# Performance work log

Hardware: AMD Instinct MI355X
Metric: run time of the kernel (lower is better)

## Reference

```python
import jax, jax.numpy as jnp
import numpy as np

S = 16          # slice count (init kwarg)
EPS = 1e-5      # BN2d default eps


def markov_sub(m, s):
    """Vectorized get_markov_sub. m: [C, C] -> [s, C, C].
    ms[i][a,b] = where(m[i,b] > 0, m[a,b], 0); mss[k] = max over rows i in slice k.
    Equivalent closed form via per-column any/all positivity of the slice rows."""
    C = m.shape[0]
    pos = (m > 0.0).reshape(s, C // s, C)          # [s, slice_size, C]
    any_p = pos.any(axis=1)[:, None, :]            # [s, 1, C]
    all_p = pos.all(axis=1)[:, None, :]            # [s, 1, C]
    mb = m[None, :, :]                             # [1, C, C]
    return jnp.where(all_p, mb,
                     jnp.where(any_p, jnp.maximum(mb, 0.0), jnp.zeros_like(mb)))


def setup_inputs() -> dict:
    key = jax.random.key(0)
    ks = jax.random.split(key, 8)
    N, C, H, W = 4, 256, 32, 32
    s = S
    feats = jax.random.normal(ks[0], (N, C, H, W), jnp.float32)
    adj_matrix = jax.random.normal(ks[1], (N, C, C), jnp.float32)
    # three 1x1 conv layers: in = S*C, out = C (stacked on leading axis)
    conv_w = jax.random.normal(ks[2], (3, C, s * C), jnp.float32) / np.sqrt(s * C).astype(np.float32)
    conv_b = jax.random.normal(ks[3], (3, C), jnp.float32) * 0.01
    bn_gamma = jnp.ones((3, C), jnp.float32)
    bn_beta = jnp.zeros((3, C), jnp.float32)
    bn_mean = jax.random.normal(ks[4], (3, C), jnp.float32) * 0.1
    bn_var = jax.random.uniform(ks[5], (3, C), jnp.float32, minval=0.5, maxval=1.5)
    return {"feats": feats, "adj_matrix": adj_matrix, "conv_w": conv_w,
            "conv_b": conv_b, "bn_gamma": bn_gamma, "bn_beta": bn_beta,
            "bn_mean": bn_mean, "bn_var": bn_var}


def reference(feats, adj_matrix, conv_w, conv_b, bn_gamma, bn_beta, bn_mean, bn_var):
    N, C, H, W = feats.shape
    s = S
    # per-sample markov sub-adjacencies, computed once and reused across layers
    mss = jax.vmap(lambda m: markov_sub(m, s))(adj_matrix)      # [N, S, C, C]
    mss = mss.reshape(N, s * C, C)                              # [N, S*C, C]
    outs = []
    x = feats
    for l in range(3):
        xp = x.reshape(N, C, H * W)                             # [N, C, HW]
        y = jnp.einsum('nkc,ncp->nkp', mss, xp)                 # sparse.mm -> [N, S*C, HW]
        y = jnp.einsum('ok,nkp->nop', conv_w[l], y) + conv_b[l][None, :, None]
        scale = (bn_gamma[l] * jax.lax.rsqrt(bn_var[l] + EPS))[None, :, None]
        y = (y - bn_mean[l][None, :, None]) * scale + bn_beta[l][None, :, None]
        y = jax.nn.relu(y).reshape(N, C, H, W)
        outs.append(y)
        x = y
    return tuple(outs)
```

## Files before the change

kernel.cpp:

```cpp
#include <hip/hip_runtime.h>
#include <stdint.h>

#define CC   256
#define SSL  16
#define NB   4
#define HWP  1024
#define K1   4096
#define EPSV 1e-5f

typedef __attribute__((ext_vector_type(8))) short bf16x8;
typedef __attribute__((ext_vector_type(4))) float f32x4;

__device__ __forceinline__ ushort f2bf(float f) {
    uint32_t u = __float_as_uint(f);
    uint32_t r = (u + 0x7FFFu + ((u >> 16) & 1u)) >> 16;
    return (ushort)r;
}

__global__ __launch_bounds__(256) void flags_kernel(const float* __restrict__ adj,
                                                    uint8_t* __restrict__ flags) {
    const int nk = blockIdx.x;
    const int n = nk >> 4, k = nk & 15;
    const int b = threadIdx.x;
    const float* m = adj + (size_t)n * CC * CC;
    bool allp = true, anyp = false;
#pragma unroll
    for (int i = 0; i < 16; ++i) {
        float v = m[(size_t)(k * 16 + i) * CC + b];
        bool p = v > 0.0f;
        allp = allp && p;
        anyp = anyp || p;
    }
    flags[(size_t)nk * CC + b] = allp ? (uint8_t)2 : (anyp ? (uint8_t)1 : (uint8_t)0);
}

__global__ __launch_bounds__(256) void convw_bf16_kernel(const float* __restrict__ w,
                                                         ushort* __restrict__ wb) {
    const int idx = (blockIdx.x * 256 + threadIdx.x) * 4;
    float4 v = *(const float4*)(w + idx);
    ushort4 o = {f2bf(v.x), f2bf(v.y), f2bf(v.z), f2bf(v.w)};
    *(ushort4*)(wb + idx) = o;
}

__global__ __launch_bounds__(256) void msst_kernel(const float* __restrict__ adj,
                                                   const uint8_t* __restrict__ flags,
                                                   ushort* __restrict__ msst) {
    const int n = blockIdx.y;
    const int at = blockIdx.x >> 2, bt = blockIdx.x & 3;
    const int a0 = at * 64, b0 = bt * 64;
    const float* m = adj + (size_t)n * CC * CC;
    __shared__ float Ms[64][68];
    __shared__ uint8_t Fl[16][64];
    const int t = threadIdx.x;
    {
        const int ar = t >> 2, bq = (t & 3) * 16;
        const float* src = m + (size_t)(a0 + ar) * CC + b0 + bq;
#pragma unroll
        for (int i = 0; i < 4; ++i)
            *(float4*)&Ms[ar][bq + i * 4] = *(const float4*)(src + i * 4);
        const int k = t >> 4, b4 = (t & 15) * 4;
        *(uchar4*)&Fl[k][b4] = *(const uchar4*)(flags + (size_t)(n * SSL + k) * CC + b0 + b4);
    }
    __syncthreads();
    const int bl = t >> 2, ac = (t & 3) * 16;
    ushort bx[16], bp[16];
#pragma unroll
    for (int i = 0; i < 16; ++i) {
        float x = Ms[ac + i][bl];
        bx[i] = f2bf(x);
        bp[i] = f2bf(fmaxf(x, 0.0f));
    }
    ushort* dst = msst + ((size_t)(n * CC + b0 + bl)) * K1 + a0 + ac;
#pragma unroll
    for (int k = 0; k < 16; ++k) {
        const uint8_t f = Fl[k][bl];
        ushort* dk = dst + k * CC;
#pragma unroll
        for (int a4 = 0; a4 < 4; ++a4) {
            ushort4 o;
            o.x = (f == 2) ? bx[a4 * 4 + 0] : ((f == 1) ? bp[a4 * 4 + 0] : (ushort)0);
            o.y = (f == 2) ? bx[a4 * 4 + 1] : ((f == 1) ? bp[a4 * 4 + 1] : (ushort)0);
            o.z = (f == 2) ? bx[a4 * 4 + 2] : ((f == 1) ? bp[a4 * 4 + 2] : (ushort)0);
            o.w = (f == 2) ? bx[a4 * 4 + 3] : ((f == 1) ? bp[a4 * 4 + 3] : (ushort)0);
            *(ushort4*)(dk + a4 * 4) = o;
        }
    }
}

__global__ __launch_bounds__(256) void featsT_kernel(const float* __restrict__ feats,
                                                     ushort* __restrict__ fT) {
    const int n = blockIdx.y;
    const int ct = blockIdx.x >> 4, pt = blockIdx.x & 15;
    const int c0 = ct * 64, p0 = pt * 64;
    const float* src = feats + ((size_t)n * CC + c0) * HWP + p0;
    __shared__ float Ts[64][68];
    const int t = threadIdx.x;
    const int cr = t >> 2, pq = (t & 3) * 16;
#pragma unroll
    for (int i = 0; i < 4; ++i)
        *(float4*)&Ts[cr][pq + i * 4] = *(const float4*)(src + (size_t)cr * HWP + pq + i * 4);
    __syncthreads();
    const int pl = t >> 2, cc0 = (t & 3) * 16;
    ushort* dst = fT + ((size_t)n * HWP + p0 + pl) * CC + c0 + cc0;
#pragma unroll
    for (int a4 = 0; a4 < 4; ++a4) {
        ushort4 o;
        o.x = f2bf(Ts[cc0 + a4 * 4 + 0][pl]);
        o.y = f2bf(Ts[cc0 + a4 * 4 + 1][pl]);
        o.z = f2bf(Ts[cc0 + a4 * 4 + 2][pl]);
        o.w = f2bf(Ts[cc0 + a4 * 4 + 3][pl]);
        *(ushort4*)(dst + a4 * 4) = o;
    }
}

__global__ __launch_bounds__(256) void weff_mfma(const ushort* __restrict__ Aw,
                                                 const ushort* __restrict__ Bm,
                                                 float* __restrict__ wpart) {
    const int tile = blockIdx.x;
    const int ln = blockIdx.y;
    const int sp = blockIdx.z;
    const int l = ln >> 2, n = ln & 3;
    const int trow = (tile >> 1) * 128, tcol = (tile & 1) * 128;
    const ushort* A = Aw + (size_t)l * CC * K1;
    const ushort* B = Bm + (size_t)n * CC * K1;
    __shared__ ushort Al[128][40];
    __shared__ ushort Bl[128][40];
    const int t = threadIdx.x;
    const int wv = t >> 6, L = t & 63;
    const int wr = (wv >> 1) * 64, wc = (wv & 1) * 64;
    const int l16 = L & 15, q = L >> 4;
    const int r0 = t >> 2, kq0 = (t & 3) * 8;
    f32x4 acc[4][4];
#pragma unroll
    for (int i = 0; i < 4; ++i)
#pragma unroll
        for (int j = 0; j < 4; ++j)
            acc[i][j] = (f32x4){0.f, 0.f, 0.f, 0.f};

    const int kbase = sp * 512;
    for (int kt = 0; kt < 16; ++kt) {
        const int kk = kbase + kt * 32;
        int4 a0 = *(const int4*)(A + (size_t)(trow + r0) * K1 + kk + kq0);
        int4 a1 = *(const int4*)(A + (size_t)(trow + 64 + r0) * K1 + kk + kq0);
        int4 b0 = *(const int4*)(B + (size_t)(tcol + r0) * K1 + kk + kq0);
        int4 b1 = *(const int4*)(B + (size_t)(tcol + 64 + r0) * K1 + kk + kq0);
        __syncthreads();
        *(int4*)&Al[r0][kq0] = a0;
        *(int4*)&Al[64 + r0][kq0] = a1;
        *(int4*)&Bl[r0][kq0] = b0;
        *(int4*)&Bl[64 + r0][kq0] = b1;
        __syncthreads();
        bf16x8 af[4], bfr[4];
#pragma unroll
        for (int i = 0; i < 4; ++i)
            af[i] = *(const bf16x8*)&Al[wr + i * 16 + l16][q * 8];
#pragma unroll
        for (int j = 0; j < 4; ++j)
            bfr[j] = *(const bf16x8*)&Bl[wc + j * 16 + l16][q * 8];
#pragma unroll
        for (int i = 0; i < 4; ++i)
#pragma unroll
            for (int j = 0; j < 4; ++j)
                acc[i][j] = __builtin_amdgcn_mfma_f32_16x16x32_bf16(af[i], bfr[j], acc[i][j], 0, 0, 0);
    }

    float* W = wpart + ((size_t)sp * 12 + ln) * (CC * CC);
#pragma unroll
    for (int i = 0; i < 4; ++i)
#pragma unroll
        for (int j = 0; j < 4; ++j) {
            const int o = trow + wr + i * 16 + q * 4;
            const int b = tcol + wc + j * 16 + l16;
#pragma unroll
            for (int r = 0; r < 4; ++r)
                W[(size_t)(o + r) * CC + b] = acc[i][j][r];
        }
}

__global__ __launch_bounds__(256) void reduce_kernel(const float* __restrict__ wpart,
                                                     const float* __restrict__ gamma,
                                                     const float* __restrict__ var,
                                                     ushort* __restrict__ Ws) {
    const int idx = (blockIdx.x * 256 + threadIdx.x) * 4;
    const int ln = idx >> 16;
    const int l = ln >> 2;
    const int o = (idx >> 8) & 255;
    float4 s = {0.f, 0.f, 0.f, 0.f};
#pragma unroll
    for (int sp = 0; sp < 8; ++sp) {
        float4 v = *(const float4*)(wpart + (size_t)sp * 12 * 65536 + idx);
        s.x += v.x; s.y += v.y; s.z += v.z; s.w += v.w;
    }
    const float sc = gamma[l * CC + o] * rsqrtf(var[l * CC + o] + EPSV);
    ushort4 ob = {f2bf(s.x * sc), f2bf(s.y * sc), f2bf(s.z * sc), f2bf(s.w * sc)};
    *(ushort4*)(Ws + idx) = ob;
}

__global__ __launch_bounds__(256) void layer_mfma(const ushort* __restrict__ xT,
                                                  const ushort* __restrict__ Wsl,
                                                  const float* __restrict__ convb_l,
                                                  const float* __restrict__ gamma_l,
                                                  const float* __restrict__ beta_l,
                                                  const float* __restrict__ mean_l,
                                                  const float* __restrict__ var_l,
                                                  float* __restrict__ outl,
                                                  ushort* __restrict__ xTn) {
    const int n = blockIdx.y;
    const int pt = blockIdx.x & 15, ot = blockIdx.x >> 4;
    const ushort* Axt = xT + (size_t)n * HWP * CC + (size_t)pt * 64 * CC;
    const ushort* Bw  = Wsl + (size_t)n * CC * CC + (size_t)ot * 64 * CC;
    __shared__ ushort Al[64][40];
    __shared__ ushort Bl[64][40];
    const int t = threadIdx.x;
    const int wv = t >> 6, L = t & 63;
    const int wr = (wv >> 1) * 32, wc = (wv & 1) * 32;
    const int l16 = L & 15, q = L >> 4;
    const int r0 = t >> 2, kq0 = (t & 3) * 8;
    f32x4 acc[2][2];
#pragma unroll
    for (int i = 0; i < 2; ++i)
#pragma unroll
        for (int j = 0; j < 2; ++j)
            acc[i][j] = (f32x4){0.f, 0.f, 0.f, 0.f};

    for (int kt = 0; kt < 8; ++kt) {
        const int kk = kt * 32;
        int4 av = *(const int4*)(Axt + (size_t)r0 * CC + kk + kq0);
        int4 bv = *(const int4*)(Bw + (size_t)r0 * CC + kk + kq0);
        __syncthreads();
        *(int4*)&Al[r0][kq0] = av;
        *(int4*)&Bl[r0][kq0] = bv;
        __syncthreads();
        bf16x8 af[2], bfr[2];
#pragma unroll
        for (int i = 0; i < 2; ++i)
            af[i] = *(const bf16x8*)&Al[wr + i * 16 + l16][q * 8];
#pragma unroll
        for (int j = 0; j < 2; ++j)
            bfr[j] = *(const bf16x8*)&Bl[wc + j * 16 + l16][q * 8];
#pragma unroll
        for (int i = 0; i < 2; ++i)
#pragma unroll
            for (int j = 0; j < 2; ++j)
                acc[i][j] = __builtin_amdgcn_mfma_f32_16x16x32_bf16(af[i], bfr[j], acc[i][j], 0, 0, 0);
    }

    float* outn = outl + (size_t)n * CC * HWP;
    ushort* xtn = xTn + (size_t)n * HWP * CC;
#pragma unroll
    for (int i = 0; i < 2; ++i)
#pragma unroll
        for (int j = 0; j < 2; ++j) {
            const int p = pt * 64 + wr + i * 16 + q * 4;
            const int o = ot * 64 + wc + j * 16 + l16;
            const float sc = gamma_l[o] * rsqrtf(var_l[o] + EPSV);
            const float b2 = sc * (convb_l[o] - mean_l[o]) + beta_l[o];
            float v0 = fmaxf(acc[i][j][0] + b2, 0.f);
            float v1 = fmaxf(acc[i][j][1] + b2, 0.f);
            float v2 = fmaxf(acc[i][j][2] + b2, 0.f);
            float v3 = fmaxf(acc[i][j][3] + b2, 0.f);
            *(float4*)(outn + (size_t)o * HWP + p) = (float4){v0, v1, v2, v3};
            xtn[(size_t)(p + 0) * CC + o] = f2bf(v0);
            xtn[(size_t)(p + 1) * CC + o] = f2bf(v1);
            xtn[(size_t)(p + 2) * CC + o] = f2bf(v2);
            xtn[(size_t)(p + 3) * CC + o] = f2bf(v3);
        }
}

extern "C" void kernel_launch(void* const* d_in, const int* in_sizes, int n_in,
                              void* d_out, int out_size, void* d_ws, size_t ws_size,
                              hipStream_t stream) {
    const float* feats  = (const float*)d_in[0];
    const float* adj    = (const float*)d_in[1];
    const float* conv_w = (const float*)d_in[2];
    const float* conv_b = (const float*)d_in[3];
    const float* gamma  = (const float*)d_in[4];
    const float* beta   = (const float*)d_in[5];
    const float* mean   = (const float*)d_in[6];
    const float* var    = (const float*)d_in[7];
    float* out = (float*)d_out;

    char* ws = (char*)d_ws;
    uint8_t* flags  = (uint8_t*)ws;
    ushort*  convwb = (ushort*)(ws + 65536);
    ushort*  msst   = (ushort*)(ws + 65536 + 6291456);
    ushort*  Wsb    = (ushort*)(ws + 65536 + 6291456 + 8388608);
    ushort*  fT0    = (ushort*)(ws + 65536 + 6291456 + 8388608 + 1572864);
    float*   wpart  = (float*)(ws + 65536 + 6291456 + 8388608 + 1572864 + 2097152);
    ushort*  xT1    = (ushort*)wpart;
    ushort*  xT2    = xT1 + (size_t)NB * HWP * CC;
    ushort*  xT3    = xT2 + (size_t)NB * HWP * CC;

    flags_kernel<<<NB * SSL, CC, 0, stream>>>(adj, flags);
    convw_bf16_kernel<<<3072, 256, 0, stream>>>(conv_w, convwb);
    msst_kernel<<<dim3(16, NB), 256, 0, stream>>>(adj, flags, msst);
    featsT_kernel<<<dim3(64, NB), 256, 0, stream>>>(feats, fT0);
    weff_mfma<<<dim3(4, 12, 8), 256, 0, stream>>>(convwb, msst, wpart);
    reduce_kernel<<<768, 256, 0, stream>>>(wpart, gamma, var, Wsb);

    const ushort* xin[3] = {fT0, xT1, xT2};
    ushort* xout[3] = {xT1, xT2, xT3};
    for (int l = 0; l < 3; ++l) {
        layer_mfma<<<dim3(64, NB), 256, 0, stream>>>(
            xin[l], Wsb + (size_t)l * NB * CC * CC,
            conv_b + l * CC, gamma + l * CC, beta + l * CC, mean + l * CC, var + l * CC,
            out + (size_t)l * NB * CC * HWP, xout[l]);
    }
}
```

Before: 131.2 us.

## Factor weight fold via max(m,0) base plus sparse correction; fuse three layers

The per-slice effective weight is rewritten as the slice-summed conv weight times relu(adj), plus a correction for columns whose slice is all-positive or all-nonpositive. Those columns are collected into an atomic badlist and fixed with a small correction GEMV. The old K=4096 split-K GEMM and its reduction pass become one K=256 MFMA. The three layer GEMMs are fused into one kernel that keeps the activations in LDS, which removes the transposed bf16 intermediates and extra launches. The cost is a memset, atomics, and a correction pass whose work depends on the data.

Measured after the change: 129.6 us. About the same (-1.2%).

```diff
diff --git a/kernel.cpp b/kernel.cpp
--- a/kernel.cpp
+++ b/kernel.cpp
@@ -2,10 +2,8 @@
 #include <stdint.h>
 
 #define CC   256
-#define SSL  16
 #define NB   4
 #define HWP  1024
-#define K1   4096
 #define EPSV 1e-5f
 
 typedef __attribute__((ext_vector_type(8))) short bf16x8;
@@ -17,40 +15,15 @@
     return (ushort)r;
 }
 
-__global__ __launch_bounds__(256) void flags_kernel(const float* __restrict__ adj,
-                                                    uint8_t* __restrict__ flags) {
-    const int nk = blockIdx.x;
-    const int n = nk >> 4, k = nk & 15;
-    const int b = threadIdx.x;
-    const float* m = adj + (size_t)n * CC * CC;
-    bool allp = true, anyp = false;
-#pragma unroll
-    for (int i = 0; i < 16; ++i) {
-        float v = m[(size_t)(k * 16 + i) * CC + b];
-        bool p = v > 0.0f;
-        allp = allp && p;
-        anyp = anyp || p;
-    }
-    flags[(size_t)nk * CC + b] = allp ? (uint8_t)2 : (anyp ? (uint8_t)1 : (uint8_t)0);
-}
-
-__global__ __launch_bounds__(256) void convw_bf16_kernel(const float* __restrict__ w,
-                                                         ushort* __restrict__ wb) {
-    const int idx = (blockIdx.x * 256 + threadIdx.x) * 4;
-    float4 v = *(const float4*)(w + idx);
-    ushort4 o = {f2bf(v.x), f2bf(v.y), f2bf(v.z), f2bf(v.w)};
-    *(ushort4*)(wb + idx) = o;
-}
-
-__global__ __launch_bounds__(256) void msst_kernel(const float* __restrict__ adj,
-                                                   const uint8_t* __restrict__ flags,
-                                                   ushort* __restrict__ msst) {
+__global__ __launch_bounds__(256) void mplusT_flags(const float* __restrict__ adj,
+                                                    ushort* __restrict__ mpT,
+                                                    unsigned int* __restrict__ count,
+                                                    unsigned int* __restrict__ badlist) {
     const int n = blockIdx.y;
     const int at = blockIdx.x >> 2, bt = blockIdx.x & 3;
     const int a0 = at * 64, b0 = bt * 64;
     const float* m = adj + (size_t)n * CC * CC;
     __shared__ float Ms[64][68];
-    __shared__ uint8_t Fl[16][64];
     const int t = threadIdx.x;
     {
         const int ar = t >> 2, bq = (t & 3) * 16;
@@ -58,157 +31,93 @@
 #pragma unroll
         for (int i = 0; i < 4; ++i)
             *(float4*)&Ms[ar][bq + i * 4] = *(const float4*)(src + i * 4);
-        const int k = t >> 4, b4 = (t & 15) * 4;
-        *(uchar4*)&Fl[k][b4] = *(const uchar4*)(flags + (size_t)(n * SSL + k) * CC + b0 + b4);
     }
     __syncthreads();
-    const int bl = t >> 2, ac = (t & 3) * 16;
-    ushort bx[16], bp[16];
-#pragma unroll
-    for (int i = 0; i < 16; ++i) {
-        float x = Ms[ac + i][bl];
-        bx[i] = f2bf(x);
-        bp[i] = f2bf(fmaxf(x, 0.0f));
-    }
-    ushort* dst = msst + ((size_t)(n * CC + b0 + bl)) * K1 + a0 + ac;
-#pragma unroll
-    for (int k = 0; k < 16; ++k) {
-        const uint8_t f = Fl[k][bl];
-        ushort* dk = dst + k * CC;
+    {
+        const int bl = t >> 2, ac = (t & 3) * 16;
+        ushort* dst = mpT + ((size_t)n * CC + b0 + bl) * CC + a0 + ac;
 #pragma unroll
         for (int a4 = 0; a4 < 4; ++a4) {
             ushort4 o;
-            o.x = (f == 2) ? bx[a4 * 4 + 0] : ((f == 1) ? bp[a4 * 4 + 0] : (ushort)0);
-            o.y = (f == 2) ? bx[a4 * 4 + 1] : ((f == 1) ? bp[a4 * 4 + 1] : (ushort)0);
-            o.z = (f == 2) ? bx[a4 * 4 + 2] : ((f == 1) ? bp[a4 * 4 + 2] : (ushort)0);
-            o.w = (f == 2) ? bx[a4 * 4 + 3] : ((f == 1) ? bp[a4 * 4 + 3] : (ushort)0);
-            *(ushort4*)(dk + a4 * 4) = o;
-        }
-    }
-}
-
-__global__ __launch_bounds__(256) void featsT_kernel(const float* __restrict__ feats,
-                                                     ushort* __restrict__ fT) {
-    const int n = blockIdx.y;
-    const int ct = blockIdx.x >> 4, pt = blockIdx.x & 15;
-    const int c0 = ct * 64, p0 = pt * 64;
-    const float* src = feats + ((size_t)n * CC + c0) * HWP + p0;
-    __shared__ float Ts[64][68];
-    const int t = threadIdx.x;
-    const int cr = t >> 2, pq = (t & 3) * 16;
-#pragma unroll
-    for (int i = 0; i < 4; ++i)
-        *(float4*)&Ts[cr][pq + i * 4] = *(const float4*)(src + (size_t)cr * HWP + pq + i * 4);
-    __syncthreads();
-    const int pl = t >> 2, cc0 = (t & 3) * 16;
-    ushort* dst = fT + ((size_t)n * HWP + p0 + pl) * CC + c0 + cc0;
-#pragma unroll
-    for (int a4 = 0; a4 < 4; ++a4) {
-        ushort4 o;
-        o.x = f2bf(Ts[cc0 + a4 * 4 + 0][pl]);
-        o.y = f2bf(Ts[cc0 + a4 * 4 + 1][pl]);
-        o.z = f2bf(Ts[cc0 + a4 * 4 + 2][pl]);
-        o.w = f2bf(Ts[cc0 + a4 * 4 + 3][pl]);
-        *(ushort4*)(dst + a4 * 4) = o;
-    }
-}
-
-__global__ __launch_bounds__(256) void weff_mfma(const ushort* __restrict__ Aw,
-                                                 const ushort* __restrict__ Bm,
-                                                 float* __restrict__ wpart) {
+            o.x = f2bf(fmaxf(Ms[ac + a4 * 4 + 0][bl], 0.f));
+            o.y = f2bf(fmaxf(Ms[ac + a4 * 4 + 1][bl], 0.f));
+            o.z = f2bf(fmaxf(Ms[ac + a4 * 4 + 2][bl], 0.f));
+            o.w = f2bf(fmaxf(Ms[ac + a4 * 4 + 3][bl], 0.f));
+            *(ushort4*)(dst + a4 * 4) = o;
+        }
+    }
+    {
+        const int kl = t >> 6, bl = t & 63;
+        bool allp = true, anyp = false;
+#pragma unroll
+        for (int i = 0; i < 16; ++i) {
+            bool p = Ms[kl * 16 + i][bl] > 0.0f;
+            allp = allp && p;
+            anyp = anyp || p;
+        }
+        const int f = allp ? 2 : (anyp ? 1 : 0);
+        if (f != 1) {
+            unsigned int pos = atomicAdd(count, 1u);
+            const int k = at * 4 + kl;
+            badlist[pos] = (unsigned int)((f << 16) | (n << 12) | (k << 8) | (b0 + bl));
+        }
+    }
+}
+
+__global__ __launch_bounds__(256) void cwsum_kernel(const float* __restrict__ w,
+                                                    ushort* __restrict__ cwS) {
+    const int idx = (blockIdx.x * 256 + threadIdx.x) * 4;
+    const int l = idx >> 16;
+    const int o = (idx >> 8) & 255;
+    const int a = idx & 255;
+    const float* src = w + (size_t)l * 1048576 + (size_t)o * 4096 + a;
+    float4 s = {0.f, 0.f, 0.f, 0.f};
+#pragma unroll
+    for (int k = 0; k < 16; ++k) {
+        float4 v = *(const float4*)(src + k * 256);
+        s.x += v.x; s.y += v.y; s.z += v.z; s.w += v.w;
+    }
+    ushort4 ob = {f2bf(s.x), f2bf(s.y), f2bf(s.z), f2bf(s.w)};
+    *(ushort4*)(cwS + idx) = ob;
+}
+
+__global__ __launch_bounds__(256) void correction_kernel(const float* __restrict__ adj,
+                                                         const float* __restrict__ conv_w,
+                                                         const unsigned int* __restrict__ count,
+                                                         const unsigned int* __restrict__ badlist,
+                                                         float* __restrict__ Wdelta) {
+    const int l = blockIdx.y;
+    const unsigned int cnt = *count;
+    __shared__ float v[256];
+    const int t = threadIdx.x;
+    for (unsigned int i = blockIdx.x; i < cnt; i += gridDim.x) {
+        const unsigned int e = badlist[i];
+        const int b = e & 255, k = (e >> 8) & 15, n = (e >> 12) & 3, f = (e >> 16) & 3;
+        __syncthreads();
+        const float mv = adj[(size_t)n * 65536 + (size_t)t * CC + b];
+        v[t] = (f == 0) ? fmaxf(mv, 0.f) : fmaxf(-mv, 0.f);
+        __syncthreads();
+        const float* cw = conv_w + (size_t)l * 1048576 + (size_t)t * 4096 + k * 256;
+        float s = 0.f;
+#pragma unroll 8
+        for (int a = 0; a < 256; ++a) s += cw[a] * v[a];
+        atomicAdd(Wdelta + (((size_t)(l * 4 + n) * 256 + t) * 256 + b), -s);
+    }
+}
+
+__global__ __launch_bounds__(256) void wbase_mfma(const ushort* __restrict__ cwS,
+                                                  const ushort* __restrict__ mpT,
+                                                  const float* __restrict__ gamma,
+                                                  const float* __restrict__ var,
+                                                  const unsigned int* __restrict__ count,
+                                                  const float* __restrict__ Wdelta,
+                                                  ushort* __restrict__ Ws) {
     const int tile = blockIdx.x;
     const int ln = blockIdx.y;
-    const int sp = blockIdx.z;
     const int l = ln >> 2, n = ln & 3;
-    const int trow = (tile >> 1) * 128, tcol = (tile & 1) * 128;
-    const ushort* A = Aw + (size_t)l * CC * K1;
-    const ushort* B = Bm + (size_t)n * CC * K1;
-    __shared__ ushort Al[128][40];
-    __shared__ ushort Bl[128][40];
-    const int t = threadIdx.x;
-    const int wv = t >> 6, L = t & 63;
-    const int wr = (wv >> 1) * 64, wc = (wv & 1) * 64;
-    const int l16 = L & 15, q = L >> 4;
-    const int r0 = t >> 2, kq0 = (t & 3) * 8;
-    f32x4 acc[4][4];
-#pragma unroll
-    for (int i = 0; i < 4; ++i)
-#pragma unroll
-        for (int j = 0; j < 4; ++j)
-            acc[i][j] = (f32x4){0.f, 0.f, 0.f, 0.f};
-
-    const int kbase = sp * 512;
-    for (int kt = 0; kt < 16; ++kt) {
-        const int kk = kbase + kt * 32;
-        int4 a0 = *(const int4*)(A + (size_t)(trow + r0) * K1 + kk + kq0);
-        int4 a1 = *(const int4*)(A + (size_t)(trow + 64 + r0) * K1 + kk + kq0);
-        int4 b0 = *(const int4*)(B + (size_t)(tcol + r0) * K1 + kk + kq0);
-        int4 b1 = *(const int4*)(B + (size_t)(tcol + 64 + r0) * K1 + kk + kq0);
-        __syncthreads();
-        *(int4*)&Al[r0][kq0] = a0;
-        *(int4*)&Al[64 + r0][kq0] = a1;
-        *(int4*)&Bl[r0][kq0] = b0;
-        *(int4*)&Bl[64 + r0][kq0] = b1;
-        __syncthreads();
-        bf16x8 af[4], bfr[4];
-#pragma unroll
-        for (int i = 0; i < 4; ++i)
-            af[i] = *(const bf16x8*)&Al[wr + i * 16 + l16][q * 8];
-#pragma unroll
-        for (int j = 0; j < 4; ++j)
-            bfr[j] = *(const bf16x8*)&Bl[wc + j * 16 + l16][q * 8];
-#pragma unroll
-        for (int i = 0; i < 4; ++i)
-#pragma unroll
-            for (int j = 0; j < 4; ++j)
-                acc[i][j] = __builtin_amdgcn_mfma_f32_16x16x32_bf16(af[i], bfr[j], acc[i][j], 0, 0, 0);
-    }
-
-    float* W = wpart + ((size_t)sp * 12 + ln) * (CC * CC);
-#pragma unroll
-    for (int i = 0; i < 4; ++i)
-#pragma unroll
-        for (int j = 0; j < 4; ++j) {
-            const int o = trow + wr + i * 16 + q * 4;
-            const int b = tcol + wc + j * 16 + l16;
-#pragma unroll
-            for (int r = 0; r < 4; ++r)
-                W[(size_t)(o + r) * CC + b] = acc[i][j][r];
-        }
-}
-
-__global__ __launch_bounds__(256) void reduce_kernel(const float* __restrict__ wpart,
-                                                     const float* __restrict__ gamma,
-                                                     const float* __restrict__ var,
-                                                     ushort* __restrict__ Ws) {
-    const int idx = (blockIdx.x * 256 + threadIdx.x) * 4;
-    const int ln = idx >> 16;
-    const int l = ln >> 2;
-    const int o = (idx >> 8) & 255;
-    float4 s = {0.f, 0.f, 0.f, 0.f};
-#pragma unroll
-    for (int sp = 0; sp < 8; ++sp) {
-        float4 v = *(const float4*)(wpart + (size_t)sp * 12 * 65536 + idx);
-        s.x += v.x; s.y += v.y; s.z += v.z; s.w += v.w;
-    }
-    const float sc = gamma[l * CC + o] * rsqrtf(var[l * CC + o] + EPSV);
-    ushort4 ob = {f2bf(s.x * sc), f2bf(s.y * sc), f2bf(s.z * sc), f2bf(s.w * sc)};
-    *(ushort4*)(Ws + idx) = ob;
-}
-
-__global__ __launch_bounds__(256) void layer_mfma(const ushort* __restrict__ xT,
-                                                  const ushort* __restrict__ Wsl,
-                                                  const float* __restrict__ convb_l,
-                                                  const float* __restrict__ gamma_l,
-                                                  const float* __restrict__ beta_l,
-                                                  const float* __restrict__ mean_l,
-                                                  const float* __restrict__ var_l,
-                                                  float* __restrict__ outl,
-                                                  ushort* __restrict__ xTn) {
-    const int n = blockIdx.y;
-    const int pt = blockIdx.x & 15, ot = blockIdx.x >> 4;
-    const ushort* Axt = xT + (size_t)n * HWP * CC + (size_t)pt * 64 * CC;
-    const ushort* Bw  = Wsl + (size_t)n * CC * CC + (size_t)ot * 64 * CC;
+    const int trow = (tile >> 2) * 64, tcol = (tile & 3) * 64;
+    const ushort* A = cwS + (size_t)l * 65536;
+    const ushort* B = mpT + (size_t)n * 65536;
     __shared__ ushort Al[64][40];
     __shared__ ushort Bl[64][40];
     const int t = threadIdx.x;
@@ -225,8 +134,8 @@
 
     for (int kt = 0; kt < 8; ++kt) {
         const int kk = kt * 32;
-        int4 av = *(const int4*)(Axt + (size_t)r0 * CC + kk + kq0);
-        int4 bv = *(const int4*)(Bw + (size_t)r0 * CC + kk + kq0);
+        int4 av = *(const int4*)(A + (size_t)(trow + r0) * CC + kk + kq0);
+        int4 bv = *(const int4*)(B + (size_t)(tcol + r0) * CC + kk + kq0);
         __syncthreads();
         *(int4*)&Al[r0][kq0] = av;
         *(int4*)&Bl[r0][kq0] = bv;
@@ -245,26 +154,93 @@
                 acc[i][j] = __builtin_amdgcn_mfma_f32_16x16x32_bf16(af[i], bfr[j], acc[i][j], 0, 0, 0);
     }
 
-    float* outn = outl + (size_t)n * CC * HWP;
-    ushort* xtn = xTn + (size_t)n * HWP * CC;
+    const unsigned int cnt = *count;
+    ushort* W = Ws + (size_t)ln * 65536;
+    const float* Wd = Wdelta + (size_t)ln * 65536;
 #pragma unroll
     for (int i = 0; i < 2; ++i)
 #pragma unroll
         for (int j = 0; j < 2; ++j) {
-            const int p = pt * 64 + wr + i * 16 + q * 4;
-            const int o = ot * 64 + wc + j * 16 + l16;
-            const float sc = gamma_l[o] * rsqrtf(var_l[o] + EPSV);
-            const float b2 = sc * (convb_l[o] - mean_l[o]) + beta_l[o];
-            float v0 = fmaxf(acc[i][j][0] + b2, 0.f);
-            float v1 = fmaxf(acc[i][j][1] + b2, 0.f);
-            float v2 = fmaxf(acc[i][j][2] + b2, 0.f);
-            float v3 = fmaxf(acc[i][j][3] + b2, 0.f);
-            *(float4*)(outn + (size_t)o * HWP + p) = (float4){v0, v1, v2, v3};
-            xtn[(size_t)(p + 0) * CC + o] = f2bf(v0);
-            xtn[(size_t)(p + 1) * CC + o] = f2bf(v1);
-            xtn[(size_t)(p + 2) * CC + o] = f2bf(v2);
-            xtn[(size_t)(p + 3) * CC + o] = f2bf(v3);
-        }
+            const int ob = trow + wr + i * 16 + q * 4;
+            const int b  = tcol + wc + j * 16 + l16;
+#pragma unroll
+            for (int r = 0; r < 4; ++r) {
+                const int o = ob + r;
+                float a = acc[i][j][r];
+                if (cnt) a += Wd[(size_t)o * CC + b];
+                const float sc = gamma[l * CC + o] * rsqrtf(var[l * CC + o] + EPSV);
+                W[(size_t)o * CC + b] = f2bf(a * sc);
+            }
+        }
+}
+
+__global__ __launch_bounds__(256) void fused_layers(const float* __restrict__ feats,
+                                                    const ushort* __restrict__ Ws,
+                                                    const float* __restrict__ conv_b,
+                                                    const float* __restrict__ gamma,
+                                                    const float* __restrict__ beta,
+                                                    const float* __restrict__ mean,
+                                                    const float* __restrict__ var,
+                                                    float* __restrict__ out) {
+    const int n = blockIdx.y;
+    const int p0 = blockIdx.x * 16;
+    __shared__ ushort xl[2][16][264];
+    const int t = threadIdx.x;
+    const int wv = t >> 6, L = t & 63;
+    const int l16 = L & 15, q = L >> 4;
+
+    {
+        const float* src = feats + ((size_t)n * CC + t) * HWP + p0;
+        float v[16];
+#pragma unroll
+        for (int i = 0; i < 4; ++i)
+            *(float4*)&v[i * 4] = *(const float4*)(src + i * 4);
+#pragma unroll
+        for (int i = 0; i < 16; ++i)
+            xl[0][i][t] = f2bf(v[i]);
+    }
+    __syncthreads();
+
+    int cur = 0;
+    for (int l = 0; l < 3; ++l) {
+        const ushort* Bw = Ws + (size_t)(l * 4 + n) * 65536;
+        f32x4 acc[4];
+#pragma unroll
+        for (int jj = 0; jj < 4; ++jj) acc[jj] = (f32x4){0.f, 0.f, 0.f, 0.f};
+
+#pragma unroll
+        for (int kt = 0; kt < 8; ++kt) {
+            const int kk = kt * 32;
+            bf16x8 af = *(const bf16x8*)&xl[cur][l16][kk + q * 8];
+#pragma unroll
+            for (int jj = 0; jj < 4; ++jj) {
+                const int o = (wv * 4 + jj) * 16 + l16;
+                bf16x8 bv = *(const bf16x8*)(Bw + (size_t)o * CC + kk + q * 8);
+                acc[jj] = __builtin_amdgcn_mfma_f32_16x16x32_bf16(af, bv, acc[jj], 0, 0, 0);
+            }
+        }
+
+        float* outn = out + (size_t)(l * 4 + n) * CC * HWP;
+#pragma unroll
+        for (int jj = 0; jj < 4; ++jj) {
+            const int o = (wv * 4 + jj) * 16 + l16;
+            const float sc = gamma[l * CC + o] * rsqrtf(var[l * CC + o] + EPSV);
+            const float b2 = sc * (conv_b[l * CC + o] - mean[l * CC + o]) + beta[l * CC + o];
+            const float v0 = fmaxf(acc[jj][0] + b2, 0.f);
+            const float v1 = fmaxf(acc[jj][1] + b2, 0.f);
+            const float v2 = fmaxf(acc[jj][2] + b2, 0.f);
+            const float v3 = fmaxf(acc[jj][3] + b2, 0.f);
+            *(float4*)(outn + (size_t)o * HWP + p0 + q * 4) = (float4){v0, v1, v2, v3};
+            if (l < 2) {
+                xl[cur ^ 1][q * 4 + 0][o] = f2bf(v0);
+                xl[cur ^ 1][q * 4 + 1][o] = f2bf(v1);
+                xl[cur ^ 1][q * 4 + 2][o] = f2bf(v2);
+                xl[cur ^ 1][q * 4 + 3][o] = f2bf(v3);
+            }
+        }
+        __syncthreads();
+        cur ^= 1;
+    }
 }
 
 extern "C" void kernel_launch(void* const* d_in, const int* in_sizes, int n_in,
@@ -281,29 +257,18 @@
     float* out = (float*)d_out;
 
     char* ws = (char*)d_ws;
-    uint8_t* flags  = (uint8_t*)ws;
-    ushort*  convwb = (ushort*)(ws + 65536);
-    ushort*  msst   = (ushort*)(ws + 65536 + 6291456);
-    ushort*  Wsb    = (ushort*)(ws + 65536 + 6291456 + 8388608);
-    ushort*  fT0    = (ushort*)(ws + 65536 + 6291456 + 8388608 + 1572864);
-    float*   wpart  = (float*)(ws + 65536 + 6291456 + 8388608 + 1572864 + 2097152);
-    ushort*  xT1    = (ushort*)wpart;
-    ushort*  xT2    = xT1 + (size_t)NB * HWP * CC;
-    ushort*  xT3    = xT2 + (size_t)NB * HWP * CC;
-
-    flags_kernel<<<NB * SSL, CC, 0, stream>>>(adj, flags);
-    convw_bf16_kernel<<<3072, 256, 0, stream>>>(conv_w, convwb);
-    msst_kernel<<<dim3(16, NB), 256, 0, stream>>>(adj, flags, msst);
-    featsT_kernel<<<dim3(64, NB), 256, 0, stream>>>(feats, fT0);
-    weff_mfma<<<dim3(4, 12, 8), 256, 0, stream>>>(convwb, msst, wpart);
-    reduce_kernel<<<768, 256, 0, stream>>>(wpart, gamma, var, Wsb);
-
-    const ushort* xin[3] = {fT0, xT1, xT2};
-    ushort* xout[3] = {xT1, xT2, xT3};
-    for (int l = 0; l < 3; ++l) {
-        layer_mfma<<<dim3(64, NB), 256, 0, stream>>>(
-            xin[l], Wsb + (size_t)l * NB * CC * CC,
-            conv_b + l * CC, gamma + l * CC, beta + l * CC, mean + l * CC, var + l * CC,
-            out + (size_t)l * NB * CC * HWP, xout[l]);
-    }
-}
+    float*        Wdelta  = (float*)ws;
+    unsigned int* count   = (unsigned int*)(ws + 3145728);
+    unsigned int* badlist = (unsigned int*)(ws + 3145792);
+    ushort*       cwS     = (ushort*)(ws + 3211328);
+    ushort*       mpT     = (ushort*)(ws + 3604544);
+    ushort*       Wsb     = (ushort*)(ws + 4128832);
+
+    hipMemsetAsync(ws, 0, 3145792, stream);
+
+    mplusT_flags<<<dim3(16, NB), 256, 0, stream>>>(adj, mpT, count, badlist);
+    cwsum_kernel<<<192, 256, 0, stream>>>(conv_w, cwS);
+    correction_kernel<<<dim3(48, 3), 256, 0, stream>>>(adj, conv_w, count, badlist, Wdelta);
+    wbase_mfma<<<dim3(16, 12), 256, 0, stream>>>(cwS, mpT, gamma, var, count, Wdelta, Wsb);
+    fused_layers<<<dim3(64, NB), 256, 0, stream>>>(feats, Wsb, conv_b, gamma, beta, mean, var, out);
+}
```
